# Optimization experiments

Hardware: AMD Instinct MI355X
Metric: run time of the kernel (lower is better)

## Reference

```python
import jax, jax.numpy as jnp
import numpy as np
import math

B, H, L, D = 4, 16, 8192, 64


def setup_inputs() -> dict:
    key = jax.random.key(0)
    kq, kk, kv, kmu = jax.random.split(key, 4)
    Q = jax.random.normal(kq, (B, H, L, D), dtype=jnp.float32)
    K = jax.random.normal(kk, (B, H, L, D), dtype=jnp.float32)
    V = jax.random.normal(kv, (B, H, L, D), dtype=jnp.float32)
    mask = jnp.ones((B, L), dtype=jnp.float32)
    # learned params (multi_gauss=True): pi init [0.5,0.5]; mu ~ N(0,0.5) with mu[0]=0
    pi = jnp.array([0.5, 0.5], dtype=jnp.float32)
    mu = jax.random.normal(kmu, (2, H, D), dtype=jnp.float32) * 0.5
    mu = mu * jnp.array([0.0, 1.0], dtype=jnp.float32)[:, None, None]
    return {"Q": Q, "K": K, "V": V, "mask": mask, "pi": pi, "mu": mu}


def reference(Q, K, V, mask, pi, mu):
    # mixture-of-Gaussian keys: shift K by two learned means, convex-combine
    p = jnp.clip(pi, 0.0, 1.0)
    K1 = K - mu[0][None, :, None, :]
    K2 = K - mu[1][None, :, None, :]
    Km = K1 * p[0] + K2 * p[1]
    # kernelized linear attention: phi(x) = elu(x)+1, scaled by 1/L^0.25
    L_ = Q.shape[2]
    s = 1.0 / math.sqrt(math.sqrt(L_))
    m = mask[:, None, :, None]  # [B,1,L,1]
    Qf = (jax.nn.elu(Q) + 1.0) * s
    Kf = (jax.nn.elu(Km) + 1.0) * m * s
    Vm = V * m
    # K^T V first: [B,H,D,D] state, then Q @ state -> [B,H,L,D]
    KV = jnp.einsum('bhld,bhle->bhde', Kf, Vm)
    return jnp.einsum('bhld,bhde->bhle', Qf, KV)
```

## Files before the change

kernel.cpp:

```cpp
#include <hip/hip_runtime.h>
#include <cstddef>
#include <stdint.h>

#define L_ 8192
#define BH_ 64
#define SCALE 0.1051120519067143f
#define SLD 72
#define NY 16

typedef __attribute__((ext_vector_type(8))) short bf16x8;
typedef __attribute__((ext_vector_type(4))) float f32x4;
typedef __attribute__((ext_vector_type(4))) unsigned short u16x4;

__device__ __forceinline__ float elu1(float x) {
    return x > 0.0f ? (x + 1.0f) : __expf(x);
}
__device__ __forceinline__ unsigned short f2bf(float x) {
    unsigned u = __float_as_uint(x);
    u += 0x7fffu + ((u >> 16) & 1u);
    return (unsigned short)(u >> 16);
}

__global__ __launch_bounds__(256) void zero_kernel(float4* __restrict__ p) {
    p[(size_t)blockIdx.x * 256 + threadIdx.x] = make_float4(0.f, 0.f, 0.f, 0.f);
}

template<bool ATOMIC>
__global__ __launch_bounds__(256, 4) void kv_kernel2(
    const float* __restrict__ K, const float* __restrict__ V,
    const float* __restrict__ mask, const float* __restrict__ pi,
    const float* __restrict__ mu, float* __restrict__ kvout)
{
    __shared__ __align__(16) unsigned short sKs[2][64 * SLD];
    __shared__ __align__(16) unsigned short sVs[2][64 * SLD];
    __shared__ float muc[64];

    const int bh = blockIdx.x;
    const int b  = bh >> 4;
    const int h  = bh & 15;
    const int l0 = blockIdx.y * (L_ / NY);
    const int t    = threadIdx.x;
    const int wave = t >> 6;
    const int lane = t & 63;
    const int r = lane & 15;
    const int q = lane >> 4;
    const int dchunk = t & 15;
    const int lquad  = t >> 4;

    const float p0 = fminf(fmaxf(pi[0], 0.f), 1.f);
    const float p1 = fminf(fmaxf(pi[1], 0.f), 1.f);
    const float psum = p0 + p1;
    if (t < 64) muc[t] = p0 * mu[h * 64 + t] + p1 * mu[1024 + h * 64 + t];

    const float* Kb = K + (size_t)bh * (L_ * 64) + (size_t)(l0 + 4 * lquad) * 64 + 4 * dchunk;
    const float* Vb = V + (size_t)bh * (L_ * 64) + (size_t)(l0 + 4 * lquad) * 64 + 4 * dchunk;
    const float* mb = mask + (size_t)b * L_ + l0 + 4 * lquad;

    const int loff = (4 * lquad) ^ ((dchunk & 3) << 3);
    const int swz  = ((r >> 2) & 3) << 3;

    f32x4 acc[4];
#pragma unroll
    for (int i = 0; i < 4; ++i) acc[i] = (f32x4){0.f, 0.f, 0.f, 0.f};

    f32x4 ka[4], va[4], kb_[4], vb_[4];
    float ma_[4], mc_[4];

#define KV_LOAD(tt, KR, VR, MR)                                              \
    {                                                                        \
        _Pragma("unroll")                                                    \
        for (int i = 0; i < 4; ++i) {                                        \
            KR[i] = *(const f32x4*)(Kb + (size_t)((tt) * 64 + i) * 64);      \
            VR[i] = *(const f32x4*)(Vb + (size_t)((tt) * 64 + i) * 64);      \
            MR[i] = mb[(tt) * 64 + i];                                       \
        }                                                                    \
    }

#define KV_STAGE(KR, VR, MR, sKp, sVp)                                       \
    {                                                                        \
        const f32x4 mm = *(const f32x4*)&muc[4 * dchunk];                    \
        float s2_[4];                                                        \
        _Pragma("unroll")                                                    \
        for (int i = 0; i < 4; ++i) s2_[i] = SCALE * MR[i] * MR[i];          \
        _Pragma("unroll")                                                    \
        for (int j = 0; j < 4; ++j) {                                        \
            u16x4 wk, wv;                                                    \
            _Pragma("unroll")                                                \
            for (int i = 0; i < 4; ++i) {                                    \
                wk[i] = f2bf(elu1(KR[i][j] * psum - mm[j]) * s2_[i]);        \
                wv[i] = f2bf(VR[i][j]);                                      \
            }                                                                \
            *(u16x4*)&sKp[(4 * dchunk + j) * SLD + loff] = wk;               \
            *(u16x4*)&sVp[(4 * dchunk + j) * SLD + loff] = wv;               \
        }                                                                    \
    }

#define KV_MFMA(sKp, sVp)                                                    \
    {                                                                        \
        const int arow = (16 * wave + r) * SLD;                              \
        const bf16x8 a0 = *(const bf16x8*)&sKp[arow + ((8 * q) ^ swz)];      \
        const bf16x8 a1 = *(const bf16x8*)&sKp[arow + 32 + ((8 * q) ^ swz)]; \
        _Pragma("unroll")                                                    \
        for (int nt = 0; nt < 4; ++nt) {                                     \
            const int brow = (16 * nt + r) * SLD;                            \
            const bf16x8 b0 = *(const bf16x8*)&sVp[brow + ((8 * q) ^ swz)];  \
            const bf16x8 b1 = *(const bf16x8*)&sVp[brow + 32 + ((8 * q) ^ swz)]; \
            acc[nt] = __builtin_amdgcn_mfma_f32_16x16x32_bf16(a0, b0, acc[nt], 0, 0, 0); \
            acc[nt] = __builtin_amdgcn_mfma_f32_16x16x32_bf16(a1, b1, acc[nt], 0, 0, 0); \
        }                                                                    \
    }

    KV_LOAD(0, ka, va, ma_);
    __syncthreads();

#pragma unroll 1
    for (int t2 = 0; t2 < 8; t2 += 2) {
        KV_LOAD(t2 + 1, kb_, vb_, mc_);
        KV_STAGE(ka, va, ma_, sKs[0], sVs[0]);
        __syncthreads();
        KV_MFMA(sKs[0], sVs[0]);
        if (t2 + 2 < 8) { KV_LOAD(t2 + 2, ka, va, ma_); }
        KV_STAGE(kb_, vb_, mc_, sKs[1], sVs[1]);
        __syncthreads();
        KV_MFMA(sKs[1], sVs[1]);
    }

    if constexpr (ATOMIC) {
        float* kvb = kvout + (size_t)bh * 4096;
#pragma unroll
        for (int nt = 0; nt < 4; ++nt)
#pragma unroll
            for (int reg = 0; reg < 4; ++reg)
                atomicAdd(kvb + (16 * wave + 4 * q + reg) * 64 + 16 * nt + r, acc[nt][reg]);
    } else {
        float* pb = kvout + ((size_t)blockIdx.y * BH_ + bh) * 4096;
#pragma unroll
        for (int nt = 0; nt < 4; ++nt)
#pragma unroll
            for (int reg = 0; reg < 4; ++reg)
                pb[(16 * wave + 4 * q + reg) * 64 + 16 * nt + r] = acc[nt][reg];
    }
#undef KV_LOAD
#undef KV_STAGE
#undef KV_MFMA
}

__global__ __launch_bounds__(256) void reduce_kernel(
    const float* __restrict__ pb, float* __restrict__ kv)
{
    const int bh = blockIdx.x;
    const size_t idx = (size_t)blockIdx.y * 1024 + (size_t)threadIdx.x * 4;
    f32x4 s = (f32x4){0.f, 0.f, 0.f, 0.f};
#pragma unroll
    for (int y = 0; y < NY; ++y)
        s += *(const f32x4*)&pb[((size_t)y * BH_ + bh) * 4096 + idx];
    *(f32x4*)&kv[(size_t)bh * 4096 + idx] = s;
}

__global__ __launch_bounds__(256) void out_kernel(
    const float* __restrict__ Q, const float* __restrict__ kv,
    float* __restrict__ out)
{
    __shared__ __align__(16) unsigned short sKVt[64 * SLD];

    const int bh = blockIdx.x;
    const int l0 = blockIdx.y * 512;
    const int t    = threadIdx.x;
    const int wave = t >> 6;
    const int lane = t & 63;
    const int r = lane & 15;
    const int q = lane >> 4;

    {
        const float* kvb = kv + (size_t)bh * 4096 + t * 16;
        const int d  = t >> 2;
        const int e0 = (t & 3) * 16;
#pragma unroll
        for (int j4 = 0; j4 < 4; ++j4) {
            const float4 f = *(const float4*)(kvb + 4 * j4);
            sKVt[(e0 + 4 * j4 + 0) * SLD + d] = f2bf(f.x);
            sKVt[(e0 + 4 * j4 + 1) * SLD + d] = f2bf(f.y);
            sKVt[(e0 + 4 * j4 + 2) * SLD + d] = f2bf(f.z);
            sKVt[(e0 + 4 * j4 + 3) * SLD + d] = f2bf(f.w);
        }
    }
    __syncthreads();

    bf16x8 bfr[4][2];
#pragma unroll
    for (int nt = 0; nt < 4; ++nt) {
        bfr[nt][0] = *(const bf16x8*)&sKVt[(16 * nt + r) * SLD + 8 * q];
        bfr[nt][1] = *(const bf16x8*)&sKVt[(16 * nt + r) * SLD + 32 + 8 * q];
    }

    const int mbase = l0 + wave * 128;
    const float* qrow = Q + (size_t)bh * (L_ * 64) + (size_t)(mbase + r) * 64 + 8 * q;
    float* ob = out + (size_t)bh * (L_ * 64);

    float4 c0 = *(const float4*)(qrow);
    float4 c1 = *(const float4*)(qrow + 4);
    float4 c2 = *(const float4*)(qrow + 32);
    float4 c3 = *(const float4*)(qrow + 36);

#pragma unroll 1
    for (int mt = 0; mt < 8; ++mt) {
        float4 n0, n1, n2, n3;
        if (mt < 7) {
            const float* nq = qrow + (size_t)(mt + 1) * 16 * 64;
            n0 = *(const float4*)(nq);
            n1 = *(const float4*)(nq + 4);
            n2 = *(const float4*)(nq + 32);
            n3 = *(const float4*)(nq + 36);
        }
        bf16x8 a0, a1;
        a0[0] = f2bf(elu1(c0.x) * SCALE); a0[1] = f2bf(elu1(c0.y) * SCALE);
        a0[2] = f2bf(elu1(c0.z) * SCALE); a0[3] = f2bf(elu1(c0.w) * SCALE);
        a0[4] = f2bf(elu1(c1.x) * SCALE); a0[5] = f2bf(elu1(c1.y) * SCALE);
        a0[6] = f2bf(elu1(c1.z) * SCALE); a0[7] = f2bf(elu1(c1.w) * SCALE);
        a1[0] = f2bf(elu1(c2.x) * SCALE); a1[1] = f2bf(elu1(c2.y) * SCALE);
        a1[2] = f2bf(elu1(c2.z) * SCALE); a1[3] = f2bf(elu1(c2.w) * SCALE);
        a1[4] = f2bf(elu1(c3.x) * SCALE); a1[5] = f2bf(elu1(c3.y) * SCALE);
        a1[6] = f2bf(elu1(c3.z) * SCALE); a1[7] = f2bf(elu1(c3.w) * SCALE);

        f32x4 acc[4];
#pragma unroll
        for (int nt = 0; nt < 4; ++nt) {
            acc[nt] = (f32x4){0.f, 0.f, 0.f, 0.f};
            acc[nt] = __builtin_amdgcn_mfma_f32_16x16x32_bf16(a0, bfr[nt][0], acc[nt], 0, 0, 0);
            acc[nt] = __builtin_amdgcn_mfma_f32_16x16x32_bf16(a1, bfr[nt][1], acc[nt], 0, 0, 0);
        }

        float* orow = ob + (size_t)(mbase + mt * 16 + 4 * q) * 64;
#pragma unroll
        for (int nt = 0; nt < 4; ++nt)
#pragma unroll
            for (int reg = 0; reg < 4; ++reg)
                orow[(size_t)reg * 64 + 16 * nt + r] = acc[nt][reg];

        c0 = n0; c1 = n1; c2 = n2; c3 = n3;
    }
}

extern "C" void kernel_launch(void* const* d_in, const int* in_sizes, int n_in,
                              void* d_out, int out_size, void* d_ws, size_t ws_size,
                              hipStream_t stream) {
    (void)in_sizes; (void)n_in; (void)out_size;
    const float* Q    = (const float*)d_in[0];
    const float* K    = (const float*)d_in[1];
    const float* V    = (const float*)d_in[2];
    const float* mask = (const float*)d_in[3];
    const float* pi   = (const float*)d_in[4];
    const float* mu   = (const float*)d_in[5];
    float* out = (float*)d_out;
    float* ws  = (float*)d_ws;

    const size_t part_floats = (size_t)NY * BH_ * 4096;
    const size_t need_bytes  = (part_floats + (size_t)BH_ * 4096) * sizeof(float);

    if (ws_size >= need_bytes) {
        float* pb  = ws;
        float* kvf = ws + part_floats;
        kv_kernel2<false><<<dim3(BH_, NY), 256, 0, stream>>>(K, V, mask, pi, mu, pb);
        reduce_kernel<<<dim3(BH_, 4), 256, 0, stream>>>(pb, kvf);
        out_kernel<<<dim3(BH_, 16), 256, 0, stream>>>(Q, kvf, out);
    } else {
        float* kvf = ws;
        zero_kernel<<<256, 256, 0, stream>>>((float4*)kvf);
        kv_kernel2<true><<<dim3(BH_, NY), 256, 0, stream>>>(K, V, mask, pi, mu, kvf);
        out_kernel<<<dim3(BH_, 16), 256, 0, stream>>>(Q, kvf, out);
    }
}
```

Before: 422.0 us.

## Load K/V directly into MFMA operand layout, dropping shared-memory staging

The KV-state kernel no longer stages bf16-converted K and V tiles through LDS with barriers. Each lane now loads the scalar K and V elements it needs straight from global memory into registers arranged as MFMA operands, double-buffered across 32-row steps. Occupancy is lowered to 3 blocks per SIMD to fit the larger register set. This removes LDS writes and reads and the __syncthreads, but swaps 16-byte vector loads for strided scalar loads. Those are coalesced only across 16 lanes of 4 bytes, and V elements are reloaded per MFMA tile, so memory efficiency may suffer.

```diff
diff --git a/kernel.cpp b/kernel.cpp
--- a/kernel.cpp
+++ b/kernel.cpp
@@ -7,10 +7,10 @@
 #define SCALE 0.1051120519067143f
 #define SLD 72
 #define NY 16
+#define NSTEP (L_ / NY / 32)
 
 typedef __attribute__((ext_vector_type(8))) short bf16x8;
 typedef __attribute__((ext_vector_type(4))) float f32x4;
-typedef __attribute__((ext_vector_type(4))) unsigned short u16x4;
 
 __device__ __forceinline__ float elu1(float x) {
     return x > 0.0f ? (x + 1.0f) : __expf(x);
@@ -26,15 +26,11 @@
 }
 
 template<bool ATOMIC>
-__global__ __launch_bounds__(256, 4) void kv_kernel2(
+__global__ __launch_bounds__(256, 3) void kv_kernel4(
     const float* __restrict__ K, const float* __restrict__ V,
     const float* __restrict__ mask, const float* __restrict__ pi,
     const float* __restrict__ mu, float* __restrict__ kvout)
 {
-    __shared__ __align__(16) unsigned short sKs[2][64 * SLD];
-    __shared__ __align__(16) unsigned short sVs[2][64 * SLD];
-    __shared__ float muc[64];
-
     const int bh = blockIdx.x;
     const int b  = bh >> 4;
     const int h  = bh & 15;
@@ -44,86 +40,71 @@
     const int lane = t & 63;
     const int r = lane & 15;
     const int q = lane >> 4;
-    const int dchunk = t & 15;
-    const int lquad  = t >> 4;
+    const int d = 16 * wave + r;
 
     const float p0 = fminf(fmaxf(pi[0], 0.f), 1.f);
     const float p1 = fminf(fmaxf(pi[1], 0.f), 1.f);
     const float psum = p0 + p1;
-    if (t < 64) muc[t] = p0 * mu[h * 64 + t] + p1 * mu[1024 + h * 64 + t];
-
-    const float* Kb = K + (size_t)bh * (L_ * 64) + (size_t)(l0 + 4 * lquad) * 64 + 4 * dchunk;
-    const float* Vb = V + (size_t)bh * (L_ * 64) + (size_t)(l0 + 4 * lquad) * 64 + 4 * dchunk;
-    const float* mb = mask + (size_t)b * L_ + l0 + 4 * lquad;
-
-    const int loff = (4 * lquad) ^ ((dchunk & 3) << 3);
-    const int swz  = ((r >> 2) & 3) << 3;
+    const float mud  = p0 * mu[h * 64 + d] + p1 * mu[1024 + h * 64 + d];
+
+    const float* Kc = K + (size_t)bh * (L_ * 64) + (size_t)(l0 + 8 * q) * 64 + d;
+    const float* Vc = V + (size_t)bh * (L_ * 64) + (size_t)(l0 + 8 * q) * 64 + r;
+    const float* mc = mask + (size_t)b * L_ + l0 + 8 * q;
 
     f32x4 acc[4];
 #pragma unroll
     for (int i = 0; i < 4; ++i) acc[i] = (f32x4){0.f, 0.f, 0.f, 0.f};
 
-    f32x4 ka[4], va[4], kb_[4], vb_[4];
-    float ma_[4], mc_[4];
-
-#define KV_LOAD(tt, KR, VR, MR)                                              \
+    float akA[8], akB[8];
+    float bvA[4][8], bvB[4][8];
+    f32x4 mkA0, mkA1, mkB0, mkB1;
+
+#define KS_LOAD(ks, AK, BV, MK0, MK1)                                        \
     {                                                                        \
         _Pragma("unroll")                                                    \
-        for (int i = 0; i < 4; ++i) {                                        \
-            KR[i] = *(const f32x4*)(Kb + (size_t)((tt) * 64 + i) * 64);      \
-            VR[i] = *(const f32x4*)(Vb + (size_t)((tt) * 64 + i) * 64);      \
-            MR[i] = mb[(tt) * 64 + i];                                       \
+        for (int j = 0; j < 8; ++j)                                          \
+            AK[j] = Kc[(size_t)(32 * (ks) + j) * 64];                        \
+        MK0 = *(const f32x4*)&mc[32 * (ks)];                                 \
+        MK1 = *(const f32x4*)&mc[32 * (ks) + 4];                             \
+        _Pragma("unroll")                                                    \
+        for (int nt = 0; nt < 4; ++nt)                                       \
+            _Pragma("unroll")                                                \
+            for (int j = 0; j < 8; ++j)                                      \
+                BV[nt][j] = Vc[(size_t)(32 * (ks) + j) * 64 + 16 * nt];      \
+    }
+
+#define KS_COMP(AK, BV, MK0, MK1)                                            \
+    {                                                                        \
+        bf16x8 af;                                                           \
+        _Pragma("unroll")                                                    \
+        for (int j = 0; j < 4; ++j) {                                        \
+            af[j]     = f2bf(elu1(AK[j] * psum - mud) *                      \
+                             (SCALE * MK0[j] * MK0[j]));                     \
+            af[j + 4] = f2bf(elu1(AK[j + 4] * psum - mud) *                  \
+                             (SCALE * MK1[j] * MK1[j]));                     \
         }                                                                    \
-    }
-
-#define KV_STAGE(KR, VR, MR, sKp, sVp)                                       \
-    {                                                                        \
-        const f32x4 mm = *(const f32x4*)&muc[4 * dchunk];                    \
-        float s2_[4];                                                        \
-        _Pragma("unroll")                                                    \
-        for (int i = 0; i < 4; ++i) s2_[i] = SCALE * MR[i] * MR[i];          \
-        _Pragma("unroll")                                                    \
-        for (int j = 0; j < 4; ++j) {                                        \
-            u16x4 wk, wv;                                                    \
+        _Pragma("unroll")                                                    \
+        for (int nt = 0; nt < 4; ++nt) {                                     \
+            bf16x8 bf_;                                                      \
             _Pragma("unroll")                                                \
-            for (int i = 0; i < 4; ++i) {                                    \
-                wk[i] = f2bf(elu1(KR[i][j] * psum - mm[j]) * s2_[i]);        \
-                wv[i] = f2bf(VR[i][j]);                                      \
-            }                                                                \
-            *(u16x4*)&sKp[(4 * dchunk + j) * SLD + loff] = wk;               \
-            *(u16x4*)&sVp[(4 * dchunk + j) * SLD + loff] = wv;               \
+            for (int j = 0; j < 8; ++j) bf_[j] = f2bf(BV[nt][j]);            \
+            acc[nt] = __builtin_amdgcn_mfma_f32_16x16x32_bf16(af, bf_, acc[nt], 0, 0, 0); \
         }                                                                    \
     }
 
-#define KV_MFMA(sKp, sVp)                                                    \
-    {                                                                        \
-        const int arow = (16 * wave + r) * SLD;                              \
-        const bf16x8 a0 = *(const bf16x8*)&sKp[arow + ((8 * q) ^ swz)];      \
-        const bf16x8 a1 = *(const bf16x8*)&sKp[arow + 32 + ((8 * q) ^ swz)]; \
-        _Pragma("unroll")                                                    \
-        for (int nt = 0; nt < 4; ++nt) {                                     \
-            const int brow = (16 * nt + r) * SLD;                            \
-            const bf16x8 b0 = *(const bf16x8*)&sVp[brow + ((8 * q) ^ swz)];  \
-            const bf16x8 b1 = *(const bf16x8*)&sVp[brow + 32 + ((8 * q) ^ swz)]; \
-            acc[nt] = __builtin_amdgcn_mfma_f32_16x16x32_bf16(a0, b0, acc[nt], 0, 0, 0); \
-            acc[nt] = __builtin_amdgcn_mfma_f32_16x16x32_bf16(a1, b1, acc[nt], 0, 0, 0); \
-        }                                                                    \
-    }
-
-    KV_LOAD(0, ka, va, ma_);
-    __syncthreads();
-
+    KS_LOAD(0, akA, bvA, mkA0, mkA1);
 #pragma unroll 1
-    for (int t2 = 0; t2 < 8; t2 += 2) {
-        KV_LOAD(t2 + 1, kb_, vb_, mc_);
-        KV_STAGE(ka, va, ma_, sKs[0], sVs[0]);
-        __syncthreads();
-        KV_MFMA(sKs[0], sVs[0]);
-        if (t2 + 2 < 8) { KV_LOAD(t2 + 2, ka, va, ma_); }
-        KV_STAGE(kb_, vb_, mc_, sKs[1], sVs[1]);
-        __syncthreads();
-        KV_MFMA(sKs[1], sVs[1]);
-    }
+    for (int ks = 0; ks < NSTEP - 2; ks += 2) {
+        KS_LOAD(ks + 1, akB, bvB, mkB0, mkB1);
+        KS_COMP(akA, bvA, mkA0, mkA1);
+        KS_LOAD(ks + 2, akA, bvA, mkA0, mkA1);
+        KS_COMP(akB, bvB, mkB0, mkB1);
+    }
+    KS_LOAD(NSTEP - 1, akB, bvB, mkB0, mkB1);
+    KS_COMP(akA, bvA, mkA0, mkA1);
+    KS_COMP(akB, bvB, mkB0, mkB1);
+#undef KS_LOAD
+#undef KS_COMP
 
     if constexpr (ATOMIC) {
         float* kvb = kvout + (size_t)bh * 4096;
@@ -140,9 +121,6 @@
             for (int reg = 0; reg < 4; ++reg)
                 pb[(16 * wave + 4 * q + reg) * 64 + 16 * nt + r] = acc[nt][reg];
     }
-#undef KV_LOAD
-#undef KV_STAGE
-#undef KV_MFMA
 }
 
 __global__ __launch_bounds__(256) void reduce_kernel(
@@ -260,13 +238,13 @@
     if (ws_size >= need_bytes) {
         float* pb  = ws;
         float* kvf = ws + part_floats;
-        kv_kernel2<false><<<dim3(BH_, NY), 256, 0, stream>>>(K, V, mask, pi, mu, pb);
+        kv_kernel4<false><<<dim3(BH_, NY), 256, 0, stream>>>(K, V, mask, pi, mu, pb);
         reduce_kernel<<<dim3(BH_, 4), 256, 0, stream>>>(pb, kvf);
         out_kernel<<<dim3(BH_, 16), 256, 0, stream>>>(Q, kvf, out);
     } else {
         float* kvf = ws;
         zero_kernel<<<256, 256, 0, stream>>>((float4*)kvf);
-        kv_kernel2<true><<<dim3(BH_, NY), 256, 0, stream>>>(K, V, mask, pi, mu, kvf);
+        kv_kernel4<true><<<dim3(BH_, NY), 256, 0, stream>>>(K, V, mask, pi, mu, kvf);
         out_kernel<<<dim3(BH_, 16), 256, 0, stream>>>(Q, kvf, out);
     }
 }
```

Result: no change. 423.8 us (+0.4%).
